# Kernel optimization log

Measured on AMD Instinct MI355X. Metric: run time of the kernel, lower is better.

Reference implementation:

```python
import jax, jax.numpy as jnp
import numpy as np

K = 3  # kernel_size


def setup_inputs() -> dict:
    key = jax.random.key(0)
    k0, k1, k2, k3, k4 = jax.random.split(key, 5)
    n, c, h, w = 16, 384, 56, 56
    G = c                      # groups defaults to in_channels
    fk = G * K * K             # filter channels = 3456
    x = jax.random.normal(k0, (n, c, h, w), jnp.float32)
    # kaiming_normal fan_out for 1x1 conv: std = sqrt(2 / fan_out), fan_out = fk
    w_conv = jax.random.normal(k1, (fk, c), jnp.float32) * np.sqrt(2.0 / fk).astype(np.float32)
    w_gate = jax.random.normal(k2, (fk, fk), jnp.float32) * 0.02
    bn_gamma = jnp.ones((fk,), jnp.float32) + 0.1 * jax.random.normal(k3, (fk,), jnp.float32)
    bn_beta = 0.1 * jax.random.normal(k4, (fk,), jnp.float32)
    bn_mean = jnp.zeros((fk,), jnp.float32)
    bn_var = jnp.ones((fk,), jnp.float32)
    return {"x": x, "w_conv": w_conv, "w_gate": w_gate, "bn_gamma": bn_gamma,
            "bn_beta": bn_beta, "bn_mean": bn_mean, "bn_var": bn_var}


def reference(x, w_conv, w_gate, bn_gamma, bn_beta, bn_mean, bn_var):
    n, c, h, w = x.shape
    G = c                     # groups = min(in_channels, c) = c
    cg = c // G               # channels per group (=1 here)
    k2 = K * K
    eps = 1e-5

    # --- dynamic filter generation branch (tiny) ---
    pooled = x.mean(axis=(2, 3))                      # [n, c]  (AdaptiveAvgPool2d(1))
    df = pooled @ w_conv.T                            # [n, G*k2] (1x1 conv)
    df = df * jax.nn.sigmoid(df @ w_gate.T)           # gated
    df = (df - bn_mean) * jax.lax.rsqrt(bn_var + eps) * bn_gamma + bn_beta  # BN (eval)
    # Softmax(dim=-2) on shape [n, G*k2, 1, 1]: the -2 axis has size 1,
    # so this yields all-ones (faithful to the original code as written).
    df = jax.nn.softmax(df[:, :, None, None], axis=-2)[:, :, 0, 0]
    filt = df.reshape(n, G, k2)                       # [n, G, k2]
    filt_c = jnp.repeat(filt, cg, axis=1)             # [n, c, k2], channel = g*cg + r

    # --- unfold-multiply-reduce (the fusion target) ---
    p = K // 2
    xp = jnp.pad(x, ((0, 0), (0, 0), (p, p), (p, p)), mode="reflect")
    # patches[p] corresponds to F.unfold kernel position p = i*K + j (row-major)
    patches = jnp.stack(
        [xp[:, :, i:i + h, j:j + w] for i in range(K) for j in range(K)], axis=0
    )                                                 # [k2, n, c, h, w]
    out = jnp.einsum("pnchw,ncp->nchw", patches, filt_c)
    return out
```

## Files before the change

kernel.cpp:

```cpp
#include <hip/hip_runtime.h>


#define HH 56
#define WW 56
#define PLANE (HH * WW)
#define NF4 (PLANE / 4)

__global__ __launch_bounds__(256)
void box3x3_reflect_v2(const float* __restrict__ x, float* __restrict__ out) {
    __shared__ float tile[PLANE];

    const long long plane = blockIdx.x;
    const float* __restrict__ xp = x + plane * (long long)PLANE;
    float* __restrict__ op = out + plane * (long long)PLANE;

    const float4* __restrict__ x4 = reinterpret_cast<const float4*>(xp);
    float4* t4 = reinterpret_cast<float4*>(tile);
    #pragma unroll
    for (int i = threadIdx.x; i < NF4; i += 256)
        t4[i] = x4[i];
    __syncthreads();

    for (int q = threadIdx.x; q < NF4; q += 256) {
        const int y = q / 14;
        const int c = (q - y * 14) * 4;

        const int ym = (y == 0)      ? 1      : y - 1;
        const int yp = (y == HH - 1) ? HH - 2 : y + 1;
        const int li = (c == 0)      ? 1      : c - 1;
        const int ri = (c == WW - 4) ? WW - 2 : c + 4;

        const float* r0 = tile + ym * WW;
        const float* r1 = tile + y  * WW;
        const float* r2 = tile + yp * WW;

        const float4 a = *reinterpret_cast<const float4*>(r0 + c);
        const float4 b = *reinterpret_cast<const float4*>(r1 + c);
        const float4 d = *reinterpret_cast<const float4*>(r2 + c);
        const float l0 = r0[li], l1 = r1[li], l2 = r2[li];
        const float e0 = r0[ri], e1 = r1[ri], e2 = r2[ri];

        float4 v;
        v.x = a.x + b.x + d.x;
        v.y = a.y + b.y + d.y;
        v.z = a.z + b.z + d.z;
        v.w = a.w + b.w + d.w;
        const float lv = l0 + l1 + l2;
        const float rv = e0 + e1 + e2;

        float4 o;
        o.x = lv  + v.x + v.y;
        o.y = v.x + v.y + v.z;
        o.z = v.y + v.z + v.w;
        o.w = v.z + v.w + rv;

        *reinterpret_cast<float4*>(op + y * WW + c) = o;
    }
}

extern "C" void kernel_launch(void* const* d_in, const int* in_sizes, int n_in,
                              void* d_out, int out_size, void* d_ws, size_t ws_size,
                              hipStream_t stream) {
    const float* x = (const float*)d_in[0];
    float* out = (float*)d_out;

    const int n_planes = out_size / PLANE;
    box3x3_reflect_v2<<<n_planes, 256, 0, stream>>>(x, out);
}
```

Before: 176.8 us.

## Replace shared-memory plane tiles with per-thread register sliding-window row strips

Drops the per-plane LDS tile and its __syncthreads. Each thread now owns a 4-column by 14-row strip and streams rows straight from global memory, keeping a rolling three-row window in registers so every input row is loaded once per strip. The grid changes from one block per plane to a flat thread grid with a bounds check. The cost is redundant halo row loads at strip edges and less contiguous global access inside a wavefront, since neighbouring row strips sit 14 rows apart.

```diff
diff --git a/kernel.cpp b/kernel.cpp
--- a/kernel.cpp
+++ b/kernel.cpp
@@ -4,49 +4,56 @@
 #define HH 56
 #define WW 56
 #define PLANE (HH * WW)
-#define NF4 (PLANE / 4)
+#define STRIPS_PER_PLANE 56
+#define ROWS_PER_STRIP 14
+
+struct Row { float4 m; float lf, rt; };
+
+__device__ __forceinline__ int refl(int y) {
+    return y < 0 ? 1 : (y > HH - 1 ? HH - 2 : y);
+}
+
+__device__ __forceinline__ Row load_row(const float* __restrict__ rp, int c, int li, int ri) {
+    Row r;
+    r.m  = *reinterpret_cast<const float4*>(rp + c);
+    r.lf = rp[li];
+    r.rt = rp[ri];
+    return r;
+}
 
 __global__ __launch_bounds__(256)
-void box3x3_reflect_v2(const float* __restrict__ x, float* __restrict__ out) {
-    __shared__ float tile[PLANE];
+void box3x3_reflect_v3(const float* __restrict__ x, float* __restrict__ out, int nthreads) {
+    const int t = blockIdx.x * 256 + threadIdx.x;
+    if (t >= nthreads) return;
 
-    const long long plane = blockIdx.x;
-    const float* __restrict__ xp = x + plane * (long long)PLANE;
-    float* __restrict__ op = out + plane * (long long)PLANE;
+    const int plane = t / STRIPS_PER_PLANE;
+    const int sub   = t - plane * STRIPS_PER_PLANE;
+    const int rs    = sub / 14;
+    const int cg    = sub - rs * 14;
+    const int c     = cg * 4;
+    const int y0    = rs * ROWS_PER_STRIP;
 
-    const float4* __restrict__ x4 = reinterpret_cast<const float4*>(xp);
-    float4* t4 = reinterpret_cast<float4*>(tile);
+    const int li = (c == 0)      ? 1      : c - 1;
+    const int ri = (c == WW - 4) ? WW - 2 : c + 4;
+
+    const float* __restrict__ xp = x   + (long long)plane * PLANE;
+    float* __restrict__       op = out + (long long)plane * PLANE;
+
+    Row a = load_row(xp + refl(y0 - 1) * WW, c, li, ri);
+    Row b = load_row(xp + y0 * WW,           c, li, ri);
+
     #pragma unroll
-    for (int i = threadIdx.x; i < NF4; i += 256)
-        t4[i] = x4[i];
-    __syncthreads();
-
-    for (int q = threadIdx.x; q < NF4; q += 256) {
-        const int y = q / 14;
-        const int c = (q - y * 14) * 4;
-
-        const int ym = (y == 0)      ? 1      : y - 1;
-        const int yp = (y == HH - 1) ? HH - 2 : y + 1;
-        const int li = (c == 0)      ? 1      : c - 1;
-        const int ri = (c == WW - 4) ? WW - 2 : c + 4;
-
-        const float* r0 = tile + ym * WW;
-        const float* r1 = tile + y  * WW;
-        const float* r2 = tile + yp * WW;
-
-        const float4 a = *reinterpret_cast<const float4*>(r0 + c);
-        const float4 b = *reinterpret_cast<const float4*>(r1 + c);
-        const float4 d = *reinterpret_cast<const float4*>(r2 + c);
-        const float l0 = r0[li], l1 = r1[li], l2 = r2[li];
-        const float e0 = r0[ri], e1 = r1[ri], e2 = r2[ri];
+    for (int i = 0; i < ROWS_PER_STRIP; ++i) {
+        const int y = y0 + i;
+        Row d = load_row(xp + refl(y + 1) * WW, c, li, ri);
 
         float4 v;
-        v.x = a.x + b.x + d.x;
-        v.y = a.y + b.y + d.y;
-        v.z = a.z + b.z + d.z;
-        v.w = a.w + b.w + d.w;
-        const float lv = l0 + l1 + l2;
-        const float rv = e0 + e1 + e2;
+        v.x = a.m.x + b.m.x + d.m.x;
+        v.y = a.m.y + b.m.y + d.m.y;
+        v.z = a.m.z + b.m.z + d.m.z;
+        v.w = a.m.w + b.m.w + d.m.w;
+        const float lv = a.lf + b.lf + d.lf;
+        const float rv = a.rt + b.rt + d.rt;
 
         float4 o;
         o.x = lv  + v.x + v.y;
@@ -55,6 +62,8 @@
         o.w = v.z + v.w + rv;
 
         *reinterpret_cast<float4*>(op + y * WW + c) = o;
+
+        a = b; b = d;
     }
 }
 
@@ -65,5 +74,7 @@
     float* out = (float*)d_out;
 
     const int n_planes = out_size / PLANE;
-    box3x3_reflect_v2<<<n_planes, 256, 0, stream>>>(x, out);
+    const int nthreads = n_planes * STRIPS_PER_PLANE;
+    const int n_blocks = (nthreads + 255) / 256;
+    box3x3_reflect_v3<<<n_blocks, 256, 0, stream>>>(x, out, nthreads);
 }
```

Measured after the change: 188.1 us. 1.06x slower.
